# Kernel optimization log

Hardware: AMD Instinct MI355X
Metric: run time of the kernel (lower is better)

Reference implementation:

```python
import jax, jax.numpy as jnp
import numpy as np

B, S, D = 8, 1024, 1024
H, DK, DV = 16, 64, 64
OUT = 64  # out_size; W_o output dim = OUT * H = 1024


def setup_inputs() -> dict:
    key = jax.random.key(0)
    ks = jax.random.split(key, 8)
    queries = jax.random.normal(ks[0], (B, S, D), dtype=jnp.float32)
    keys = jax.random.normal(ks[1], (B, S, D), dtype=jnp.float32)
    values = jax.random.normal(ks[2], (B, S, D), dtype=jnp.float32)
    # Linear weights stored as [in, out] (no bias per bias=False)
    Wq = jax.random.normal(ks[3], (D, DK * H), dtype=jnp.float32) * 0.02
    Wk = jax.random.normal(ks[4], (D, DK * H), dtype=jnp.float32) * 0.02
    Wv = jax.random.normal(ks[5], (D, DV * H), dtype=jnp.float32) * 0.02
    Wo = jax.random.normal(ks[6], (DV * H, OUT * H), dtype=jnp.float32) * 0.02
    valid_lens = jax.random.randint(ks[7], (B,), 1, S + 1, dtype=jnp.int32)
    return {"queries": queries, "keys": keys, "values": values,
            "Wq": Wq, "Wk": Wk, "Wv": Wv, "Wo": Wo, "valid_lens": valid_lens}


def reference(queries, keys, values, Wq, Wk, Wv, Wo, valid_lens):
    b, s, _ = queries.shape
    # projections + transpose_qkv: [B,S,H*dh] -> [B,H,S,dh]
    q = (queries @ Wq).reshape(b, s, H, DK).transpose(0, 2, 1, 3)
    k = (keys @ Wk).reshape(b, keys.shape[1], H, DK).transpose(0, 2, 1, 3)
    v = (values @ Wv).reshape(b, values.shape[1], H, DV).transpose(0, 2, 1, 3)
    scale = DK ** 0.5  # epsilon = 0.0
    scores = jnp.einsum('bhqd,bhkd->bhqk', q, k) / scale
    # valid_lens masking on last axis: masked entries set to -1e6 (not -inf)
    kv_len = k.shape[2]
    mask = jnp.arange(kv_len)[None, None, None, :] < valid_lens[:, None, None, None]
    scores = jnp.where(mask, scores, -1e6)
    attn = jax.nn.softmax(scores, axis=-1)  # dropout p=0.0 -> identity
    out = jnp.einsum('bhqk,bhkd->bhqd', attn, v)
    # transpose_output: [B,H,S,dv] -> [B,S,H*dv]
    out = out.transpose(0, 2, 1, 3).reshape(b, s, H * DV)
    return out @ Wo
```

## Files before the change

### kernel.cpp

```cpp
#include <hip/hip_runtime.h>
#include <hip/hip_bf16.h>
#include <stdint.h>

typedef __bf16 bf16_t;
typedef __bf16 bf16x8 __attribute__((ext_vector_type(8)));
typedef float f32x4 __attribute__((ext_vector_type(4)));

#define B_  8
#define S_  1024
#define D_  1024
#define H_  16
#define DH_ 64

static __device__ __forceinline__ f32x4 mfma_bf16(bf16x8 a, bf16x8 b, f32x4 c) {
  return __builtin_amdgcn_mfma_f32_16x16x32_bf16(a, b, c, 0, 0, 0);
}

#define GLOAD_LDS16(g, l)                                                     \
  __builtin_amdgcn_global_load_lds(                                           \
      (const __attribute__((address_space(1))) void*)(g),                     \
      (__attribute__((address_space(3))) void*)(l), 16, 0, 0)

__global__ __launch_bounds__(256) void transpose4(
    const float* __restrict__ w0, const float* __restrict__ w1,
    const float* __restrict__ w2, const float* __restrict__ w3,
    bf16_t* __restrict__ t0, bf16_t* __restrict__ t1,
    bf16_t* __restrict__ t2, bf16_t* __restrict__ t3)
{
  __shared__ float tile[64][65];
  const float* src; bf16_t* dst;
  switch (blockIdx.z) {
    case 0: src = w0; dst = t0; break;
    case 1: src = w1; dst = t1; break;
    case 2: src = w2; dst = t2; break;
    default: src = w3; dst = t3; break;
  }
  const int tx = threadIdx.x & 63;
  const int ty = threadIdx.x >> 6;
  const int c0 = blockIdx.x * 64, r0 = blockIdx.y * 64;
#pragma unroll
  for (int r = ty; r < 64; r += 4)
    tile[r][tx] = src[(size_t)(r0 + r) * 1024 + c0 + tx];
  __syncthreads();
#pragma unroll
  for (int r = ty; r < 64; r += 4)
    dst[(size_t)(c0 + r) * 1024 + r0 + tx] = (bf16_t)tile[tx][r];
}

__global__ __launch_bounds__(256) void convert_qkv(
    const float* __restrict__ q, const float* __restrict__ k,
    const float* __restrict__ v,
    bf16_t* __restrict__ qo, bf16_t* __restrict__ ko, bf16_t* __restrict__ vo)
{
  const float* src; bf16_t* dst;
  switch (blockIdx.y) {
    case 0: src = q; dst = qo; break;
    case 1: src = k; dst = ko; break;
    default: src = v; dst = vo; break;
  }
  const size_t i = ((size_t)blockIdx.x * 256 + threadIdx.x) * 8;
  float4 a = *(const float4*)(src + i);
  float4 b = *(const float4*)(src + i + 4);
  bf16x8 o;
  o[0] = (bf16_t)a.x; o[1] = (bf16_t)a.y; o[2] = (bf16_t)a.z; o[3] = (bf16_t)a.w;
  o[4] = (bf16_t)b.x; o[5] = (bf16_t)b.y; o[6] = (bf16_t)b.z; o[7] = (bf16_t)b.w;
  *(bf16x8*)(dst + i) = o;
}

__global__ __launch_bounds__(256) void transposeV(
    const bf16_t* __restrict__ src, bf16_t* __restrict__ dst)
{
  __shared__ bf16_t t[64 * 72];
  const size_t base = (size_t)blockIdx.y * (64 * 1024);
  const int s0 = blockIdx.x * 64;
#pragma unroll
  for (int it = 0; it < 2; ++it) {
    const int c = it * 256 + threadIdx.x;
    const int r = c >> 3, col8 = (c & 7) * 8;
    bf16x8 v = *(const bf16x8*)(src + base + (size_t)(s0 + r) * 64 + col8);
    *(bf16x8*)(t + r * 72 + col8) = v;
  }
  __syncthreads();
#pragma unroll
  for (int it = 0; it < 2; ++it) {
    const int c = it * 256 + threadIdx.x;
    const int d = c >> 3, sc8 = (c & 7) * 8;
    bf16x8 v;
#pragma unroll
    for (int j = 0; j < 8; ++j) v[j] = t[(sc8 + j) * 72 + d];
    *(bf16x8*)(dst + base + (size_t)d * 1024 + s0 + sc8) = v;
  }
}

#define BM_G 256
#define BN_G 128
#define BK_G 64
#define KDIM 1024
#define NK_G (KDIM / BK_G)
#define ATILE (BM_G * BK_G)
#define BTILE (BN_G * BK_G)
#define LDS_BYTES ((3 * (ATILE + BTILE)) * 2)

template <int MODE>
__device__ __forceinline__ void gemm_core(
    const bf16_t* __restrict__ Ap, const bf16_t* __restrict__ Bp,
    void* __restrict__ Cp, bf16_t* smem)
{
  bf16_t* const As = smem;
  bf16_t* const Bs = smem + 3 * ATILE;

  const int tid  = threadIdx.x;
  const int wv   = tid >> 6;
  const int lane = tid & 63;
  const int wm   = wv >> 1;
  const int wn   = wv & 1;
  const int quad = lane >> 4;
  const int l15  = lane & 15;

  const int tileN = blockIdx.x & 7;
  const int tileM = blockIdx.x >> 3;

  const int lr  = lane >> 3;
  const int swz = (((lane & 7) ^ lr) << 3);
  const bf16_t* gA0 = Ap + (size_t)(tileM * BM_G + wv * 8 + lr) * KDIM + swz;
  const bf16_t* gB0 = Bp + (size_t)(tileN * BN_G + wv * 8 + lr) * KDIM + swz;
  const int lA0 = wv * 8 * BK_G;
  const int lB0 = wv * 8 * BK_G;

#define STAGE_TILE(koff, bA, bB) do {                                          \
    GLOAD_LDS16(gA0 + (koff),                       As + (bA) + lA0);          \
    GLOAD_LDS16(gA0 + (size_t)64  * KDIM + (koff),  As + (bA) + lA0 + 64*BK_G); \
    GLOAD_LDS16(gA0 + (size_t)128 * KDIM + (koff),  As + (bA) + lA0 + 128*BK_G);\
    GLOAD_LDS16(gA0 + (size_t)192 * KDIM + (koff),  As + (bA) + lA0 + 192*BK_G);\
    GLOAD_LDS16(gB0 + (koff),                       Bs + (bB) + lB0);          \
    GLOAD_LDS16(gB0 + (size_t)64  * KDIM + (koff),  Bs + (bB) + lB0 + 64*BK_G); \
  } while (0)

  f32x4 acc[4][4];
#pragma unroll
  for (int mi = 0; mi < 4; ++mi)
#pragma unroll
    for (int ni = 0; ni < 4; ++ni)
      acc[mi][ni] = (f32x4){0.f, 0.f, 0.f, 0.f};

  STAGE_TILE(0, 0, 0);
  STAGE_TILE(BK_G, ATILE, BTILE);

  int cbA = 0, cbB = 0;
  int sbA = 2 * ATILE, sbB = 2 * BTILE;

  for (int t = 0; t < NK_G; ++t) {
    if (t + 2 < NK_G) STAGE_TILE((size_t)(t + 2) * BK_G, sbA, sbB);

    if (t < NK_G - 2)       asm volatile("s_waitcnt vmcnt(12)" ::: "memory");
    else if (t == NK_G - 2) asm volatile("s_waitcnt vmcnt(6)" ::: "memory");
    else                    asm volatile("s_waitcnt vmcnt(0)" ::: "memory");
    __builtin_amdgcn_s_barrier();
    asm volatile("" ::: "memory");

    bf16x8 af[2][4], bfr[2][4];
#pragma unroll
    for (int kk = 0; kk < 2; ++kk) {
      const int sl = (((quad + (kk << 2)) ^ (l15 & 7)) << 3);
#pragma unroll
      for (int mi = 0; mi < 4; ++mi)
        af[kk][mi] = *(const bf16x8*)(As + cbA + (wm * 64 + mi * 16 + l15) * BK_G + sl);
#pragma unroll
      for (int ni = 0; ni < 4; ++ni)
        bfr[kk][ni] = *(const bf16x8*)(Bs + cbB + (wn * 64 + ni * 16 + l15) * BK_G + sl);
    }
    __builtin_amdgcn_s_setprio(1);
#pragma unroll
    for (int kk = 0; kk < 2; ++kk)
#pragma unroll
      for (int mi = 0; mi < 4; ++mi)
#pragma unroll
        for (int ni = 0; ni < 4; ++ni)
          acc[mi][ni] = mfma_bf16(af[kk][mi], bfr[kk][ni], acc[mi][ni]);
    __builtin_amdgcn_s_setprio(0);

    asm volatile("" ::: "memory");
    __builtin_amdgcn_s_barrier();

    cbA += ATILE; if (cbA == 3 * ATILE) cbA = 0;
    cbB += BTILE; if (cbB == 3 * BTILE) cbB = 0;
    sbA += ATILE; if (sbA == 3 * ATILE) sbA = 0;
    sbB += BTILE; if (sbB == 3 * BTILE) sbB = 0;
  }
#undef STAGE_TILE

#pragma unroll
  for (int mi = 0; mi < 4; ++mi) {
#pragma unroll
    for (int ni = 0; ni < 4; ++ni) {
#pragma unroll
      for (int r = 0; r < 4; ++r) {
        const int row = tileM * BM_G + wm * 64 + mi * 16 + quad * 4 + r;
        const int col = tileN * BN_G + wn * 64 + ni * 16 + l15;
        if (MODE == 0) {
          ((float*)Cp)[(size_t)row * 1024 + col] = acc[mi][ni][r];
        } else {
          const int b = row >> 10, s = row & 1023;
          const int h = col >> 6,  d = col & 63;
          ((bf16_t*)Cp)[(((size_t)(b * H_ + h) << 10) | s) * DH_ + d] =
              (bf16_t)acc[mi][ni][r];
        }
      }
    }
  }
}

__global__ __launch_bounds__(512, 2) void gemm_proj(
    const bf16_t* __restrict__ A0, const bf16_t* __restrict__ A1, const bf16_t* __restrict__ A2,
    const bf16_t* __restrict__ B0, const bf16_t* __restrict__ B1, const bf16_t* __restrict__ B2,
    bf16_t* __restrict__ C0, bf16_t* __restrict__ C1, bf16_t* __restrict__ C2)
{
  extern __shared__ bf16_t smem[];
  const bf16_t* Ap; const bf16_t* Bp; bf16_t* Cp;
  if (blockIdx.z == 0)      { Ap = A0; Bp = B0; Cp = C0; }
  else if (blockIdx.z == 1) { Ap = A1; Bp = B1; Cp = C1; }
  else                      { Ap = A2; Bp = B2; Cp = C2; }
  gemm_core<1>(Ap, Bp, (void*)Cp, smem);
}

__global__ __launch_bounds__(512, 2) void gemm_out(
    const bf16_t* __restrict__ Ap, const bf16_t* __restrict__ Bp,
    float* __restrict__ Cp)
{
  extern __shared__ bf16_t smem[];
  gemm_core<0>(Ap, Bp, (void*)Cp, smem);
}

__global__ __launch_bounds__(256) void attn64(
    const bf16_t* __restrict__ Q,
    const bf16_t* __restrict__ Kv,
    const bf16_t* __restrict__ Vt,
    const int* __restrict__ valid_lens,
    bf16_t* __restrict__ O)
{
  const int h  = blockIdx.x;
  const int qt = blockIdx.y;
  const int b  = blockIdx.z;
  const int tid  = threadIdx.x;
  const int wave = tid >> 6;
  const int lane = tid & 63;
  const int quad = lane >> 4;
  const int l15  = lane & 15;

  const int L   = valid_lens[b];
  const int nkt = (L + 63) >> 6;

  const size_t base = ((size_t)(b * H_ + h)) * S_ * DH_;
  const bf16_t* Qp = Q  + base;
  const bf16_t* Kp = Kv + base;
  const bf16_t* Vp = Vt + base;

  __shared__ bf16_t KsA[64 * 32];
  __shared__ bf16_t KsB[64 * 32];
  __shared__ bf16_t VsA[64 * 32];
  __shared__ bf16_t VsB[64 * 32];
  __shared__ bf16_t Pb[4][16 * 72];
  bf16_t* const Pw = &Pb[wave][0];

  const int sr = tid >> 2;
  const int sj = (tid & 3) << 3;
  const int ldsOff = (wave * 64) * 8;

  const int qrow = qt * 64 + wave * 16 + l15;
  const bf16x8 qf0 = *(const bf16x8*)(Qp + (size_t)qrow * DH_ + quad * 8);
  const bf16x8 qf1 = *(const bf16x8*)(Qp + (size_t)qrow * DH_ + 32 + quad * 8);

  f32x4 o[4];
  float lsum[4];
#pragma unroll
  for (int r = 0; r < 4; ++r) {
    o[r] = (f32x4){0.f, 0.f, 0.f, 0.f};
    lsum[r] = 0.f;
  }

  for (int kt = 0; kt < nkt; ++kt) {
    const int k0 = kt * 64;

    __syncthreads();
    GLOAD_LDS16(Kp + (size_t)(k0 + sr) * DH_ + sj,      KsA + ldsOff);
    GLOAD_LDS16(Kp + (size_t)(k0 + sr) * DH_ + 32 + sj, KsB + ldsOff);
    GLOAD_LDS16(Vp + (size_t)sr * S_ + k0 + sj,         VsA + ldsOff);
    GLOAD_LDS16(Vp + (size_t)sr * S_ + k0 + 32 + sj,    VsB + ldsOff);
    __syncthreads();

    f32x4 sc[4];
#pragma unroll
    for (int n16 = 0; n16 < 4; ++n16) {
      const int row = (n16 * 16 + l15) * 32 + quad * 8;
      bf16x8 kf0 = *(const bf16x8*)(KsA + row);
      bf16x8 kf1 = *(const bf16x8*)(KsB + row);
      f32x4 s = (f32x4){0.f, 0.f, 0.f, 0.f};
      s = mfma_bf16(qf0, kf0, s);
      s = mfma_bf16(qf1, kf1, s);
      sc[n16] = s;
    }

    if (k0 + 64 <= L) {
#pragma unroll
      for (int n16 = 0; n16 < 4; ++n16) {
#pragma unroll
        for (int r = 0; r < 4; ++r) {
          const float p = __expf(sc[n16][r] * 0.125f);
          lsum[r] += p;
          Pw[(quad * 4 + r) * 72 + n16 * 16 + l15] = (bf16_t)p;
        }
      }
    } else {
#pragma unroll
      for (int n16 = 0; n16 < 4; ++n16) {
        const bool valid = (k0 + n16 * 16 + l15) < L;
#pragma unroll
        for (int r = 0; r < 4; ++r) {
          const float p = valid ? __expf(sc[n16][r] * 0.125f) : 0.f;
          lsum[r] += p;
          Pw[(quad * 4 + r) * 72 + n16 * 16 + l15] = (bf16_t)p;
        }
      }
    }

    const bf16x8 pf0 = *(const bf16x8*)(Pw + l15 * 72 + quad * 8);
    const bf16x8 pf1 = *(const bf16x8*)(Pw + l15 * 72 + 32 + quad * 8);
#pragma unroll
    for (int dt = 0; dt < 4; ++dt) {
      const int row = (dt * 16 + l15) * 32 + quad * 8;
      bf16x8 vf0 = *(const bf16x8*)(VsA + row);
      bf16x8 vf1 = *(const bf16x8*)(VsB + row);
      o[dt] = mfma_bf16(pf0, vf0, o[dt]);
      o[dt] = mfma_bf16(pf1, vf1, o[dt]);
    }
  }

  float inv[4];
#pragma unroll
  for (int r = 0; r < 4; ++r) {
    float t = lsum[r];
    t += __shfl_xor(t, 1, 64);
    t += __shfl_xor(t, 2, 64);
    t += __shfl_xor(t, 4, 64);
    t += __shfl_xor(t, 8, 64);
    inv[r] = 1.f / t;
  }
  const int qout = qt * 64 + wave * 16 + quad * 4;
#pragma unroll
  for (int dt = 0; dt < 4; ++dt) {
#pragma unroll
    for (int r = 0; r < 4; ++r) {
      const float v = o[dt][r] * inv[r];
      O[((size_t)(b * S_ + qout + r)) * (H_ * DH_) + h * DH_ + dt * 16 + l15] = (bf16_t)v;
    }
  }
}

extern "C" void kernel_launch(void* const* d_in, const int* in_sizes, int n_in,
                              void* d_out, int out_size, void* d_ws, size_t ws_size,
                              hipStream_t stream) {
  const float* queries = (const float*)d_in[0];
  const float* keys    = (const float*)d_in[1];
  const float* values  = (const float*)d_in[2];
  const float* Wq      = (const float*)d_in[3];
  const float* Wk      = (const float*)d_in[4];
  const float* Wv      = (const float*)d_in[5];
  const float* Wo      = (const float*)d_in[6];
  const int* valid_lens = (const int*)d_in[7];
  float* out = (float*)d_out;

  bf16_t* ws = (bf16_t*)d_ws;
  const size_t MB = 1024 * 1024;
  bf16_t* WqT = ws + 0 * MB;
  bf16_t* WkT = ws + 1 * MB;
  bf16_t* WvT = ws + 2 * MB;
  bf16_t* WoT = ws + 3 * MB;
  bf16_t* Qc  = ws + 4 * MB;
  bf16_t* Kc  = ws + 12 * MB;
  bf16_t* Vc  = ws + 20 * MB;
  bf16_t* Qb  = ws + 28 * MB;
  bf16_t* Kb  = ws + 36 * MB;
  bf16_t* Vb  = ws + 44 * MB;
  bf16_t* VbT = ws + 52 * MB;
  bf16_t* Ab  = ws + 60 * MB;

  (void)hipFuncSetAttribute((const void*)gemm_proj,
                            hipFuncAttributeMaxDynamicSharedMemorySize, LDS_BYTES);
  (void)hipFuncSetAttribute((const void*)gemm_out,
                            hipFuncAttributeMaxDynamicSharedMemorySize, LDS_BYTES);

  transpose4<<<dim3(16, 16, 4), 256, 0, stream>>>(Wq, Wk, Wv, Wo, WqT, WkT, WvT, WoT);

  convert_qkv<<<dim3(4096, 3), 256, 0, stream>>>(queries, keys, values, Qc, Kc, Vc);

  gemm_proj<<<dim3(256, 1, 3), 512, LDS_BYTES, stream>>>(Qc, Kc, Vc,
                                                         WqT, WkT, WvT,
                                                         Qb, Kb, Vb);

  transposeV<<<dim3(16, 128), 256, 0, stream>>>(Vb, VbT);

  attn64<<<dim3(16, 16, 8), 256, 0, stream>>>(Qb, Kb, VbT, valid_lens, Ab);

  gemm_out<<<dim3(256, 1, 1), 512, LDS_BYTES, stream>>>(Ab, WoT, out);
}
```

Before: 303.9 us.

## Use 256x256 GEMM tiles with double buffering and XCD-aware tile mapping

Enlarges the GEMM block tile from 256x128 to 256x256, with each wave computing 128x64 in two MFMA halves, and replaces the triple-buffered LDS ring with double buffering. The QKV projections become one flat launch that treats the three inputs and weights as contiguous segments, and block indices are mapped so that each XCD gets neighbouring M tiles. The aim is more operand reuse per LDS load, fewer blocks and better L2 locality. In exchange it needs more accumulator registers, leaves less prefetch depth, and relies on the Qc/Kc/Vc, weight and output buffers sitting at fixed contiguous offsets.

```diff
diff --git a/kernel.cpp b/kernel.cpp
--- a/kernel.cpp
+++ b/kernel.cpp
@@ -93,82 +93,80 @@
 }
 
 #define BM_G 256
-#define BN_G 128
+#define BN_G 256
 #define BK_G 64
 #define KDIM 1024
 #define NK_G (KDIM / BK_G)
-#define ATILE (BM_G * BK_G)
-#define BTILE (BN_G * BK_G)
-#define LDS_BYTES ((3 * (ATILE + BTILE)) * 2)
+#define TILE_EL (BM_G * BK_G)
+#define LDS_BYTES (2 * 2 * TILE_EL * 2)
 
 template <int MODE>
 __device__ __forceinline__ void gemm_core(
-    const bf16_t* __restrict__ Ap, const bf16_t* __restrict__ Bp,
-    void* __restrict__ Cp, bf16_t* smem)
+    const bf16_t* __restrict__ Ap,
+    const bf16_t* __restrict__ Bp,
+    void* __restrict__ Cp,
+    bf16_t* smem, int tileM, int tileMloc, int tileN)
 {
   bf16_t* const As = smem;
-  bf16_t* const Bs = smem + 3 * ATILE;
+  bf16_t* const Bs = smem + 2 * TILE_EL;
 
   const int tid  = threadIdx.x;
   const int wv   = tid >> 6;
   const int lane = tid & 63;
-  const int wm   = wv >> 1;
-  const int wn   = wv & 1;
+  const int wm   = wv >> 2;
+  const int wn   = wv & 3;
   const int quad = lane >> 4;
   const int l15  = lane & 15;
-
-  const int tileN = blockIdx.x & 7;
-  const int tileM = blockIdx.x >> 3;
 
   const int lr  = lane >> 3;
   const int swz = (((lane & 7) ^ lr) << 3);
   const bf16_t* gA0 = Ap + (size_t)(tileM * BM_G + wv * 8 + lr) * KDIM + swz;
   const bf16_t* gB0 = Bp + (size_t)(tileN * BN_G + wv * 8 + lr) * KDIM + swz;
-  const int lA0 = wv * 8 * BK_G;
-  const int lB0 = wv * 8 * BK_G;
-
-#define STAGE_TILE(koff, bA, bB) do {                                          \
-    GLOAD_LDS16(gA0 + (koff),                       As + (bA) + lA0);          \
-    GLOAD_LDS16(gA0 + (size_t)64  * KDIM + (koff),  As + (bA) + lA0 + 64*BK_G); \
-    GLOAD_LDS16(gA0 + (size_t)128 * KDIM + (koff),  As + (bA) + lA0 + 128*BK_G);\
-    GLOAD_LDS16(gA0 + (size_t)192 * KDIM + (koff),  As + (bA) + lA0 + 192*BK_G);\
-    GLOAD_LDS16(gB0 + (koff),                       Bs + (bB) + lB0);          \
-    GLOAD_LDS16(gB0 + (size_t)64  * KDIM + (koff),  Bs + (bB) + lB0 + 64*BK_G); \
+  const int lOff = wv * 512;
+
+#define STAGE8(koff, buf) do {                                                  \
+    GLOAD_LDS16(gA0 + (koff),                       As + (buf)*TILE_EL + 0*4096 + lOff); \
+    GLOAD_LDS16(gA0 + (size_t)64  * KDIM + (koff),  As + (buf)*TILE_EL + 1*4096 + lOff); \
+    GLOAD_LDS16(gA0 + (size_t)128 * KDIM + (koff),  As + (buf)*TILE_EL + 2*4096 + lOff); \
+    GLOAD_LDS16(gA0 + (size_t)192 * KDIM + (koff),  As + (buf)*TILE_EL + 3*4096 + lOff); \
+    GLOAD_LDS16(gB0 + (koff),                       Bs + (buf)*TILE_EL + 0*4096 + lOff); \
+    GLOAD_LDS16(gB0 + (size_t)64  * KDIM + (koff),  Bs + (buf)*TILE_EL + 1*4096 + lOff); \
+    GLOAD_LDS16(gB0 + (size_t)128 * KDIM + (koff),  Bs + (buf)*TILE_EL + 2*4096 + lOff); \
+    GLOAD_LDS16(gB0 + (size_t)192 * KDIM + (koff),  Bs + (buf)*TILE_EL + 3*4096 + lOff); \
   } while (0)
 
-  f32x4 acc[4][4];
-#pragma unroll
-  for (int mi = 0; mi < 4; ++mi)
+  f32x4 acc[8][4];
+#pragma unroll
+  for (int mi = 0; mi < 8; ++mi)
 #pragma unroll
     for (int ni = 0; ni < 4; ++ni)
       acc[mi][ni] = (f32x4){0.f, 0.f, 0.f, 0.f};
 
-  STAGE_TILE(0, 0, 0);
-  STAGE_TILE(BK_G, ATILE, BTILE);
-
-  int cbA = 0, cbB = 0;
-  int sbA = 2 * ATILE, sbB = 2 * BTILE;
+  STAGE8(0, 0);
+  STAGE8(BK_G, 1);
+  asm volatile("s_waitcnt vmcnt(8)" ::: "memory");
+  __builtin_amdgcn_s_barrier();
 
   for (int t = 0; t < NK_G; ++t) {
-    if (t + 2 < NK_G) STAGE_TILE((size_t)(t + 2) * BK_G, sbA, sbB);
-
-    if (t < NK_G - 2)       asm volatile("s_waitcnt vmcnt(12)" ::: "memory");
-    else if (t == NK_G - 2) asm volatile("s_waitcnt vmcnt(6)" ::: "memory");
-    else                    asm volatile("s_waitcnt vmcnt(0)" ::: "memory");
-    __builtin_amdgcn_s_barrier();
-    asm volatile("" ::: "memory");
-
-    bf16x8 af[2][4], bfr[2][4];
+    const int cb = (t & 1) * TILE_EL;
+
+    bf16x8 bfr[2][4], af[2][4];
 #pragma unroll
     for (int kk = 0; kk < 2; ++kk) {
       const int sl = (((quad + (kk << 2)) ^ (l15 & 7)) << 3);
 #pragma unroll
+      for (int ni = 0; ni < 4; ++ni)
+        bfr[kk][ni] = *(const bf16x8*)(Bs + cb + (wn * 64 + ni * 16 + l15) * BK_G + sl);
+    }
+#pragma unroll
+    for (int kk = 0; kk < 2; ++kk) {
+      const int sl = (((quad + (kk << 2)) ^ (l15 & 7)) << 3);
+#pragma unroll
       for (int mi = 0; mi < 4; ++mi)
-        af[kk][mi] = *(const bf16x8*)(As + cbA + (wm * 64 + mi * 16 + l15) * BK_G + sl);
-#pragma unroll
-      for (int ni = 0; ni < 4; ++ni)
-        bfr[kk][ni] = *(const bf16x8*)(Bs + cbB + (wn * 64 + ni * 16 + l15) * BK_G + sl);
-    }
+        af[kk][mi] = *(const bf16x8*)(As + cb + (wm * 128 + mi * 16 + l15) * BK_G + sl);
+    }
+    asm volatile("s_waitcnt lgkmcnt(0)" ::: "memory");
+    __builtin_amdgcn_sched_barrier(0);
     __builtin_amdgcn_s_setprio(1);
 #pragma unroll
     for (int kk = 0; kk < 2; ++kk)
@@ -178,24 +176,48 @@
         for (int ni = 0; ni < 4; ++ni)
           acc[mi][ni] = mfma_bf16(af[kk][mi], bfr[kk][ni], acc[mi][ni]);
     __builtin_amdgcn_s_setprio(0);
+#pragma unroll
+    for (int kk = 0; kk < 2; ++kk) {
+      const int sl = (((quad + (kk << 2)) ^ (l15 & 7)) << 3);
+#pragma unroll
+      for (int mi = 0; mi < 4; ++mi)
+        af[kk][mi] = *(const bf16x8*)(As + cb + (wm * 128 + 64 + mi * 16 + l15) * BK_G + sl);
+    }
+    asm volatile("s_waitcnt lgkmcnt(0)" ::: "memory");
+    __builtin_amdgcn_sched_barrier(0);
+    __builtin_amdgcn_s_setprio(1);
+#pragma unroll
+    for (int kk = 0; kk < 2; ++kk)
+#pragma unroll
+      for (int mi = 0; mi < 4; ++mi)
+#pragma unroll
+        for (int ni = 0; ni < 4; ++ni)
+          acc[4 + mi][ni] = mfma_bf16(af[kk][mi], bfr[kk][ni], acc[4 + mi][ni]);
+    __builtin_amdgcn_s_setprio(0);
 
     asm volatile("" ::: "memory");
     __builtin_amdgcn_s_barrier();
 
-    cbA += ATILE; if (cbA == 3 * ATILE) cbA = 0;
-    cbB += BTILE; if (cbB == 3 * BTILE) cbB = 0;
-    sbA += ATILE; if (sbA == 3 * ATILE) sbA = 0;
-    sbB += BTILE; if (sbB == 3 * BTILE) sbB = 0;
-  }
-#undef STAGE_TILE
-
-#pragma unroll
-  for (int mi = 0; mi < 4; ++mi) {
+    if (t < NK_G - 2) {
+      STAGE8((size_t)(t + 2) * BK_G, t & 1);
+      asm volatile("s_waitcnt vmcnt(8)" ::: "memory");
+    } else if (t == NK_G - 2) {
+      asm volatile("s_waitcnt vmcnt(0)" ::: "memory");
+    }
+    if (t < NK_G - 1) {
+      asm volatile("" ::: "memory");
+      __builtin_amdgcn_s_barrier();
+    }
+  }
+#undef STAGE8
+
+#pragma unroll
+  for (int mi = 0; mi < 8; ++mi) {
 #pragma unroll
     for (int ni = 0; ni < 4; ++ni) {
 #pragma unroll
       for (int r = 0; r < 4; ++r) {
-        const int row = tileM * BM_G + wm * 64 + mi * 16 + quad * 4 + r;
+        const int row = tileMloc * BM_G + wm * 128 + mi * 16 + quad * 4 + r;
         const int col = tileN * BN_G + wn * 64 + ni * 16 + l15;
         if (MODE == 0) {
           ((float*)Cp)[(size_t)row * 1024 + col] = acc[mi][ni][r];
@@ -211,16 +233,17 @@
 }
 
 __global__ __launch_bounds__(512, 2) void gemm_proj(
-    const bf16_t* __restrict__ A0, const bf16_t* __restrict__ A1, const bf16_t* __restrict__ A2,
-    const bf16_t* __restrict__ B0, const bf16_t* __restrict__ B1, const bf16_t* __restrict__ B2,
-    bf16_t* __restrict__ C0, bf16_t* __restrict__ C1, bf16_t* __restrict__ C2)
+    const bf16_t* __restrict__ A, const bf16_t* __restrict__ Bw,
+    bf16_t* __restrict__ Cb)
 {
   extern __shared__ bf16_t smem[];
-  const bf16_t* Ap; const bf16_t* Bp; bf16_t* Cp;
-  if (blockIdx.z == 0)      { Ap = A0; Bp = B0; Cp = C0; }
-  else if (blockIdx.z == 1) { Ap = A1; Bp = B1; Cp = C1; }
-  else                      { Ap = A2; Bp = B2; Cp = C2; }
-  gemm_core<1>(Ap, Bp, (void*)Cp, smem);
+  const int xcd = blockIdx.x & 7;
+  const int r   = blockIdx.x >> 3;
+  const int tileN = r & 3;
+  const int tileM = xcd * 12 + (r >> 2);
+  const int seg = tileM >> 5;
+  gemm_core<1>(A, Bw + ((size_t)seg << 20), (void*)(Cb + ((size_t)seg << 23)),
+               smem, tileM, tileM & 31, tileN);
 }
 
 __global__ __launch_bounds__(512, 2) void gemm_out(
@@ -228,7 +251,11 @@
     float* __restrict__ Cp)
 {
   extern __shared__ bf16_t smem[];
-  gemm_core<0>(Ap, Bp, (void*)Cp, smem);
+  const int xcd = blockIdx.x & 7;
+  const int r   = blockIdx.x >> 3;
+  const int tileN = r & 3;
+  const int tileM = xcd * 4 + (r >> 2);
+  gemm_core<0>(Ap, Bp, (void*)Cp, smem, tileM, tileM, tileN);
 }
 
 __global__ __launch_bounds__(256) void attn64(
@@ -393,13 +420,11 @@
 
   convert_qkv<<<dim3(4096, 3), 256, 0, stream>>>(queries, keys, values, Qc, Kc, Vc);
 
-  gemm_proj<<<dim3(256, 1, 3), 512, LDS_BYTES, stream>>>(Qc, Kc, Vc,
-                                                         WqT, WkT, WvT,
-                                                         Qb, Kb, Vb);
+  gemm_proj<<<dim3(384, 1, 1), 512, LDS_BYTES, stream>>>(Qc, WqT, Qb);
 
   transposeV<<<dim3(16, 128), 256, 0, stream>>>(Vb, VbT);
 
   attn64<<<dim3(16, 16, 8), 256, 0, stream>>>(Qb, Kb, VbT, valid_lens, Ab);
 
-  gemm_out<<<dim3(256, 1, 1), 512, LDS_BYTES, stream>>>(Ab, WoT, out);
-}
+  gemm_out<<<dim3(128, 1, 1), 512, LDS_BYTES, stream>>>(Ab, WoT, out);
+}
```

Measured after the change: 308.6 us. About the same (+1.5%).
